# Kernel optimization log

Measured on AMD Instinct MI355X. Metric: run time of the kernel, lower is better.

Reference implementation:

```python
import jax, jax.numpy as jnp
import numpy as np
from jax import lax

PI = float(np.pi)
K_TOP = 128
N_BINS = 64

def _normalize(x, axis, eps=1e-12):
    n = jnp.sqrt(jnp.sum(x * x, axis=axis, keepdims=True))
    return x / jnp.maximum(n, eps)

def _conv(x, w, b):
    y = lax.conv_general_dilated(x, w, (1, 1), 'SAME',
                                 dimension_numbers=('NCHW', 'OIHW', 'NCHW'))
    return y + b[None, :, None, None]

def _maxpool2(x):
    return lax.reduce_window(x, -jnp.inf, lax.max, (1, 1, 2, 2), (1, 1, 2, 2), 'VALID')

def setup_inputs() -> dict:
    key = jax.random.key(0)
    ks = jax.random.split(key, 12)
    B, C, H, W = 16, 1, 512, 512
    PD, NPT = 128, 64
    fc_in = NPT + 64 * 4 * 4 + 3  # 1091
    def lin_init(k, fan_in, shape):
        bound = 1.0 / np.sqrt(fan_in)
        return jax.random.uniform(k, shape, jnp.float32, -bound, bound)
    return {
        'image': jax.random.normal(ks[0], (B, C, H, W), jnp.float32),
        'pattern_receptors': jax.random.normal(ks[1], (NPT, PD), jnp.float32) * 0.1,
        'conv1_w': lin_init(ks[2], 2 * 9, (32, 2, 3, 3)),
        'conv1_b': lin_init(ks[3], 2 * 9, (32,)),
        'conv2_w': lin_init(ks[4], 32 * 9, (64, 32, 3, 3)),
        'conv2_b': lin_init(ks[5], 32 * 9, (64,)),
        'fc1_w': lin_init(ks[6], fc_in, (512, fc_in)),
        'fc1_b': lin_init(ks[7], fc_in, (512,)),
        'fc2_w': lin_init(ks[8], 512, (PD, 512)),
        'fc2_b': lin_init(ks[9], 512, (PD,)),
        'ln_g': jnp.ones((PD,), jnp.float32),
        'ln_b': jnp.zeros((PD,), jnp.float32),
    }

def reference(image, pattern_receptors, conv1_w, conv1_b, conv2_w, conv2_b,
              fc1_w, fc1_b, fc2_w, fc2_b, ln_g, ln_b):
    B, C, H, W = image.shape
    # ---- frequency domain ----
    freq = jnp.fft.fft2(image, axes=(2, 3))
    magnitude = jnp.abs(freq)
    phase = jnp.angle(freq)
    # ---- pattern matching (topk of FFT magnitude vs receptor library) ----
    flat_mag = magnitude.reshape(B, C, -1)
    dom, _ = lax.top_k(flat_mag, K_TOP)          # [B, C, 128]
    dom = dom.reshape(B, -1)                     # [B, C*128]
    sims = jnp.matmul(_normalize(dom, 1), _normalize(pattern_receptors, 1).T)  # [B, 64]
    # ---- spatial path (original detaches via numpy roundtrip) ----
    img = lax.stop_gradient(image)
    gy = jnp.gradient(img, axis=2)
    gx = jnp.gradient(img, axis=3)
    gmag = jnp.sqrt(gx * gx + gy * gy)
    gori = jnp.arctan2(gy, gx)
    spat_in = jnp.stack([gmag, gori], axis=2).reshape(B, 2 * C, H, W)
    h = jax.nn.relu(_conv(spat_in, conv1_w, conv1_b))
    h = _maxpool2(h)                             # [B,32,H/2,W/2]
    h = jax.nn.relu(_conv(h, conv2_w, conv2_b))  # [B,64,H/2,W/2]
    Hp, Wp = h.shape[2], h.shape[3]
    h = h.reshape(B, 64, 4, Hp // 4, 4, Wp // 4).mean(axis=(3, 5))  # adaptive avg 4x4
    spatial = h.reshape(B, -1)                   # [B, 1024]
    # ---- phase statistics ----
    pf = phase.reshape(B, -1)
    p_mean = jnp.mean(pf, axis=1)
    p_std = jnp.std(pf, axis=1, ddof=1)
    bins = jnp.clip(jnp.floor((pf + PI) / (2 * PI) * N_BINS), 0, N_BINS - 1).astype(jnp.int32)
    hist = jnp.zeros((B, N_BINS), jnp.float32).at[jnp.arange(B)[:, None], bins].add(1.0)
    hist = hist / jnp.sum(hist, axis=1, keepdims=True)
    p_ent = -jnp.sum(hist * jnp.log(hist + 1e-10), axis=1)
    phase_feats = jnp.stack([p_mean, p_std, p_ent], axis=1)  # [B, 3]
    # ---- fuse: MLP + LayerNorm ----
    combined = jnp.concatenate([sims, spatial, phase_feats], axis=1)  # [B, 1091]
    z = jax.nn.relu(combined @ fc1_w.T + fc1_b)
    z = z @ fc2_w.T + fc2_b
    mu = jnp.mean(z, axis=-1, keepdims=True)
    var = jnp.var(z, axis=-1, keepdims=True)
    holo = (z - mu) / jnp.sqrt(var + 1e-5) * ln_g + ln_b
    return sims, spatial, phase_feats, holo
```

## Files before the change

kernel.cpp:

```cpp
#include <hip/hip_runtime.h>
#include <hip/hip_fp16.h>
#include <math.h>


#define PI_F 3.14159274f
#define TWO_PI_F 6.28318548f

typedef _Float16 half8 __attribute__((ext_vector_type(8)));
typedef float floatx4 __attribute__((ext_vector_type(4)));

#define OFF_BIG   8388608
#define OFF_SMALL 25165824
#define NBIN 2048

__global__ void __launch_bounds__(256) init_kernel(float* __restrict__ zp,
                                                   float2* __restrict__ tw,
                                                   const float* __restrict__ w2,
                                                   const float* __restrict__ w1,
                                                   _Float16* __restrict__ wrep,
                                                   _Float16* __restrict__ w1r) {
    int idx = blockIdx.x * 256 + threadIdx.x;
    if (idx < 82992) zp[idx] = 0.0f;
    if (idx < 512) {
        if (idx == 0) tw[0] = make_float2(1.f, 0.f);
        else {
            int h = 31 - __clz(idx);
            int H = 1 << h;
            float sn, cs;
            sincosf(-PI_F * (float)(idx - H) / (float)H, &sn, &cs);
            tw[idx] = make_float2(cs, sn);
        }
    }
    if (idx < 18432) {
        int j = idx & 7;
        int lane = (idx >> 3) & 63;
        int nt = (idx >> 9) & 3;
        int tap = idx >> 11;
        int oc = nt * 16 + (lane & 15);
        int ic = (lane >> 4) * 8 + j;
        wrep[idx] = (_Float16)w2[(oc * 32 + ic) * 9 + tap];
    }
    if (idx < 1024) {
        int j = idx & 7;
        int lane = (idx >> 3) & 63;
        int nt = idx >> 9;
        int oc = nt * 16 + (lane & 15);
        int k = (lane >> 4) * 8 + j;
        _Float16 v = (_Float16)0.f;
        if (k < 18) {
            int tap = k >> 1, ch = k & 1;
            v = (_Float16)w1[oc * 18 + ch * 9 + tap];
        }
        w1r[idx] = v;
    }
}

__global__ void __launch_bounds__(256) fft_rows(const float* __restrict__ img,
                                                const float2* __restrict__ twg,
                                                float2* __restrict__ rowfft) {
    __shared__ float2 s[512];
    __shared__ float2 tw[512];
    const int t = threadIdx.x;
    const int row = blockIdx.x;
    const float* x = img + (long long)row * 512;

    for (int i = t; i < 512; i += 256) tw[i] = twg[i];
    for (int i = t; i < 512; i += 256) s[i] = make_float2(x[i], 0.f);
    __syncthreads();
#pragma unroll
    for (int st = 9; st >= 1; --st) {
        const int half = 1 << (st - 1);
        const int pos = t & (half - 1);
        const int grp = t >> (st - 1);
        const int i1 = (grp << st) + pos;
        const int i2 = i1 + half;
        float2 w = tw[half + pos];
        float2 a = s[i1], b = s[i2];
        float dx = a.x - b.x, dy = a.y - b.y;
        s[i1] = make_float2(a.x + b.x, a.y + b.y);
        s[i2] = make_float2(dx * w.x - dy * w.y, dx * w.y + dy * w.x);
        __syncthreads();
    }
    for (int i = t; i < 512; i += 256) rowfft[(long long)row * 512 + i] = s[i];
}

__global__ void __launch_bounds__(256) fft_cols(const float2* __restrict__ rowfft,
                                                const float2* __restrict__ twg,
                                                float* __restrict__ magT,
                                                float* __restrict__ psum,
                                                float* __restrict__ psumsq,
                                                unsigned* __restrict__ phist,
                                                unsigned* __restrict__ mhist) {
    __shared__ float2 s[8 * 512];
    __shared__ float2 tw[512];
    __shared__ unsigned ph[64];
    __shared__ unsigned mh[NBIN];
    __shared__ float red[8];
    const int t = threadIdx.x;
    const int b = blockIdx.x >> 6;
    const int x0 = (blockIdx.x & 63) * 8;

    for (int i = t; i < 512; i += 256) tw[i] = twg[i];
    if (t < 64) ph[t] = 0u;
    for (int i = t; i < NBIN; i += 256) mh[i] = 0u;
    for (int idx = t; idx < 8 * 512; idx += 256) {
        int y = idx >> 3;
        int c = idx & 7;
        s[c * 512 + y] = rowfft[((long long)(b * 512 + y)) * 512 + x0 + c];
    }
    __syncthreads();

    const int c = t >> 5;
    const int j0 = t & 31;
    float2* sc = s + c * 512;
#pragma unroll
    for (int st = 9; st >= 1; --st) {
        const int half = 1 << (st - 1);
#pragma unroll
        for (int k = 0; k < 8; ++k) {
            int j = j0 + (k << 5);
            int pos = j & (half - 1);
            int grp = j >> (st - 1);
            int i1 = (grp << st) + pos;
            int i2 = i1 + half;
            float2 w = tw[half + pos];
            float2 a = sc[i1], bb = sc[i2];
            float dx = a.x - bb.x, dy = a.y - bb.y;
            sc[i1] = make_float2(a.x + bb.x, a.y + bb.y);
            sc[i2] = make_float2(dx * w.x - dy * w.y, dx * w.y + dy * w.x);
        }
        __syncthreads();
    }

    float lsum = 0.f, lsq = 0.f;
    for (int idx = t; idx < 8 * 512; idx += 256) {
        int cc = idx >> 9;
        int y = idx & 511;
        float2 v = s[cc * 512 + y];
        float mag = sqrtf(v.x * v.x + v.y * v.y);
        magT[((long long)(b * 512 + x0 + cc)) * 512 + y] = mag;
        unsigned mb = min(__float_as_uint(mag) >> 20, (unsigned)(NBIN - 1));
        atomicAdd(&mh[mb], 1u);
        float phv = atan2f(v.y, v.x);
        lsum += phv;
        lsq += phv * phv;
        int bin = (int)floorf((phv + PI_F) / TWO_PI_F * 64.0f);
        bin = min(max(bin, 0), 63);
        atomicAdd(&ph[bin], 1u);
    }
    for (int off = 32; off > 0; off >>= 1) {
        lsum += __shfl_down(lsum, off);
        lsq  += __shfl_down(lsq, off);
    }
    if ((t & 63) == 0) { red[t >> 6] = lsum; red[4 + (t >> 6)] = lsq; }
    __syncthreads();
    if (t == 0) {
        atomicAdd(psum + b,   red[0] + red[1] + red[2] + red[3]);
        atomicAdd(psumsq + b, red[4] + red[5] + red[6] + red[7]);
    }
    if (t < 64 && ph[t]) atomicAdd(&phist[b * 64 + t], ph[t]);
    for (int i = t; i < NBIN; i += 256)
        if (mh[i]) atomicAdd(&mhist[b * NBIN + i], mh[i]);
}

__global__ void __launch_bounds__(256) thresh_kernel(const unsigned* __restrict__ mhist,
                                                     int* __restrict__ selbin) {
    __shared__ unsigned csum[256];
    const int b = blockIdx.x, t = threadIdx.x;
    unsigned s = 0;
    for (int i = 0; i < NBIN / 256; ++i) s += mhist[b * NBIN + t * (NBIN / 256) + i];
    csum[t] = s;
    __syncthreads();
    if (t == 0) {
        unsigned acc = 0; int chunk = 0;
        for (int i = 255; i >= 0; --i) {
            acc += csum[i];
            if (acc >= 128u) { chunk = i; break; }
        }
        unsigned acc2 = acc - csum[chunk];
        int tb = chunk * (NBIN / 256);
        for (int i = chunk * (NBIN / 256) + (NBIN / 256) - 1; i >= chunk * (NBIN / 256); --i) {
            acc2 += mhist[b * NBIN + i];
            if (acc2 >= 128u) { tb = i; break; }
        }
        selbin[b] = tb;
    }
}

#define TK_CAP 4096
__global__ void __launch_bounds__(256) collect_kernel(const float* __restrict__ magT,
                                                      const int* __restrict__ selbin,
                                                      float* __restrict__ cand,
                                                      unsigned* __restrict__ ccnt) {
    const int blk = blockIdx.x;
    const int b = blk >> 4, chunk = blk & 15;
    const unsigned tb = (unsigned)selbin[b];
    const floatx4* m = (const floatx4*)(magT + (long long)b * 262144 + chunk * 16384);
    float* cb = cand + b * TK_CAP;
    for (int i = threadIdx.x; i < 4096; i += 256) {
        floatx4 v = m[i];
#pragma unroll
        for (int k = 0; k < 4; ++k) {
            float x = v[k];
            unsigned bin = min(__float_as_uint(x) >> 20, (unsigned)(NBIN - 1));
            if (bin >= tb) {
                unsigned p = atomicAdd(&ccnt[b], 1u);
                if (p < TK_CAP) cb[p] = x;
            }
        }
    }
}

__global__ void __launch_bounds__(1024) sort_kernel(const float* __restrict__ cand,
                                                    const unsigned* __restrict__ ccnt,
                                                    float* __restrict__ dom) {
    __shared__ float c[TK_CAP];
    const int b = blockIdx.x, t = threadIdx.x;
    const unsigned n = min(ccnt[b], (unsigned)TK_CAP);
    int P = 256;
    while (P < (int)n) P <<= 1;
    for (int i = t; i < P; i += 1024) c[i] = (i < (int)n) ? cand[b * TK_CAP + i] : -1.0f;
    __syncthreads();
    for (int k = 2; k <= P; k <<= 1) {
        for (int j = k >> 1; j > 0; j >>= 1) {
            for (int i = t; i < P; i += 1024) {
                int ixj = i ^ j;
                if (ixj > i) {
                    float a = c[i], d = c[ixj];
                    bool up = ((i & k) == 0);
                    if (up ? (a < d) : (a > d)) { c[i] = d; c[ixj] = a; }
                }
            }
            __syncthreads();
        }
    }
    if (t < 128) dom[b * 128 + t] = c[t];
}

__global__ void __launch_bounds__(256) sims_kernel(const float* __restrict__ dom,
                                                   const float* __restrict__ rec,
                                                   float* __restrict__ comb,
                                                   float* __restrict__ dout) {
    __shared__ float sd[16 * 128];
    __shared__ float sr[64 * 128];
    __shared__ float scale[80];
    const int t = threadIdx.x;
    for (int i = t; i < 2048; i += 256) sd[i] = dom[i];
    for (int i = t; i < 8192; i += 256) sr[i] = rec[i];
    __syncthreads();
    if (t < 80) {
        const float* base = (t < 16) ? (sd + t * 128) : (sr + (t - 16) * 128);
        float s = 0.f;
        for (int k = 0; k < 128; ++k) s += base[k] * base[k];
        scale[t] = 1.0f / fmaxf(sqrtf(s), 1e-12f);
    }
    __syncthreads();
    for (int o = t; o < 1024; o += 256) {
        int b = o >> 6, p = o & 63;
        const float* dv = sd + b * 128;
        const float* rv = sr + p * 128;
        float s = 0.f;
        for (int k = 0; k < 128; ++k) s += dv[k] * rv[k];
        float val = s * scale[b] * scale[16 + p];
        dout[b * 64 + p] = val;
        comb[b * 1091 + p] = val;
    }
}

__global__ void __launch_bounds__(256) grad_conv1_mfma(const float* __restrict__ img,
                                                       const half8* __restrict__ w1r,
                                                       const float* __restrict__ c1b,
                                                       _Float16* __restrict__ h1) {
    __shared__ float simg[36 * 37];
    __shared__ _Float16 sgrad[(34 * 36 + 1) * 2];
    const int blk = blockIdx.x;
    const int b = blk >> 8;
    const int tr = blk & 255;
    const int TY = (tr >> 4) * 32, TX = (tr & 15) * 32;
    const int t = threadIdx.x;
    const float* im = img + (long long)b * 262144;

    for (int idx = t; idx < 1296; idx += 256) {
        int iy = idx / 36, ix = idx - iy * 36;
        int gy = min(max(TY - 2 + iy, 0), 511);
        int gx = min(max(TX - 2 + ix, 0), 511);
        simg[iy * 37 + ix] = im[gy * 512 + gx];
    }
    if (t == 0) { sgrad[2448] = (_Float16)0.f; sgrad[2449] = (_Float16)0.f; }
    __syncthreads();

    for (int idx = t; idx < 1156; idx += 256) {
        int ly = idx / 34, lx = idx - ly * 34;
        int gy = TY - 1 + ly, gx = TX - 1 + lx;
        float up = simg[ly * 37 + lx + 1];
        float dn = simg[(ly + 2) * 37 + lx + 1];
        float lf = simg[(ly + 1) * 37 + lx];
        float rt = simg[(ly + 1) * 37 + lx + 2];
        float fy = (gy <= 0 || gy >= 511) ? 1.f : 0.5f;
        float fx = (gx <= 0 || gx >= 511) ? 1.f : 0.5f;
        float gyv = (dn - up) * fy, gxv = (rt - lf) * fx;
        bool inside = ((unsigned)gy < 512u) && ((unsigned)gx < 512u);
        float mag = inside ? sqrtf(gxv * gxv + gyv * gyv) : 0.f;
        float ori = inside ? atan2f(gyv, gxv) : 0.f;
        int p = (ly * 36 + lx) * 2;
        sgrad[p] = (_Float16)mag;
        sgrad[p + 1] = (_Float16)ori;
    }
    __syncthreads();

    const int w = t >> 6, lane = t & 63;
    const int q = lane >> 4, m = lane & 15;
    const int oc0 = m, oc1 = 16 + m;
    const float bias0 = c1b[oc0], bias1 = c1b[oc1];
    half8 Bf0 = w1r[lane], Bf1 = w1r[64 + lane];
    const unsigned* gp = (const unsigned*)sgrad;
    const int ZP = 1224;

    const int sy = (m >> 1) & 1, sx = m & 1, dqx = m >> 2;

#pragma unroll 4
    for (int i = 0; i < 16; ++i) {
        const int mt = w * 16 + i;
        const int qy = mt >> 2, qxg = mt & 3;
        const int py = 2 * qy + sy;
        const int px = 2 * (qxg * 4 + dqx) + sx;
        const int base = py * 36 + px;

        int o0 = (q == 0) ? base      : (q == 1) ? base + 37 : (q == 2) ? base + 74 : ZP;
        int o1 = (q == 0) ? base + 1  : (q == 1) ? base + 38 : ZP;
        int o2 = (q == 0) ? base + 2  : (q == 1) ? base + 72 : ZP;
        int o3 = (q == 0) ? base + 36 : (q == 1) ? base + 73 : ZP;

        union { unsigned u[4]; half8 h; } Af;
        Af.u[0] = gp[o0]; Af.u[1] = gp[o1]; Af.u[2] = gp[o2]; Af.u[3] = gp[o3];

        floatx4 acc0 = {bias0, bias0, bias0, bias0};
        floatx4 acc1 = {bias1, bias1, bias1, bias1};
        acc0 = __builtin_amdgcn_mfma_f32_16x16x32_f16(Af.h, Bf0, acc0, 0, 0, 0);
        acc1 = __builtin_amdgcn_mfma_f32_16x16x32_f16(Af.h, Bf1, acc1, 0, 0, 0);

        float v0 = fmaxf(fmaxf(acc0[0], acc0[1]), fmaxf(acc0[2], acc0[3]));
        float v1 = fmaxf(fmaxf(acc1[0], acc1[1]), fmaxf(acc1[2], acc1[3]));
        v0 = fmaxf(v0, 0.f);
        v1 = fmaxf(v1, 0.f);

        const int PY = (TY >> 1) + qy;
        const int PX = (TX >> 1) + qxg * 4 + q;
        _Float16* dst = h1 + (((size_t)(b * 256 + PY)) * 256 + PX) * 32;
        dst[oc0] = (_Float16)v0;
        dst[oc1] = (_Float16)v1;
    }
}

__global__ void __launch_bounds__(256) conv2_mfma(const _Float16* __restrict__ h1,
                                                  const _Float16* __restrict__ wrep,
                                                  const float* __restrict__ c2b,
                                                  float* __restrict__ sacc) {
    __shared__ _Float16 tile[18 * 34 * 32];
    __shared__ float lsum[64];
    const int blk = blockIdx.x;
    const int b  = blk >> 7;
    const int yt = (blk >> 3) & 15;
    const int xt = blk & 7;
    const int y0 = yt * 16, x0 = xt * 32;
    const int t = threadIdx.x;
    if (t < 64) lsum[t] = 0.f;

    for (int c = t; c < 18 * 136; c += 256) {
        int row = c / 136;
        int chunk = c - row * 136;
        int gy = y0 - 1 + row;
        int px = chunk >> 2;
        int gx = x0 - 1 + px;
        floatx4 v = {0.f, 0.f, 0.f, 0.f};
        if ((unsigned)gy < 256u && (unsigned)gx < 256u)
            v = *(const floatx4*)(h1 + (((size_t)(b * 256 + gy)) * 256 + gx) * 32 + (chunk & 3) * 8);
        *(floatx4*)(tile + (row * 34 + px) * 32 + (chunk & 3) * 8) = v;
    }
    __syncthreads();

    const int w = t >> 6, lane = t & 63;
    const int q = lane >> 4, ln15 = lane & 15;
    float bias[4];
#pragma unroll
    for (int nt = 0; nt < 4; ++nt) bias[nt] = c2b[nt * 16 + ln15];
    float partial[4] = {0.f, 0.f, 0.f, 0.f};

#pragma unroll 1
    for (int gr = 0; gr < 2; ++gr) {
        floatx4 acc[4][4];
#pragma unroll
        for (int mt = 0; mt < 4; ++mt)
#pragma unroll
            for (int nt = 0; nt < 4; ++nt)
                acc[mt][nt] = floatx4{bias[nt], bias[nt], bias[nt], bias[nt]};

        const _Float16* ab = tile + (((w * 4 + gr * 2) * 34) + ln15) * 32 + q * 8;
        const _Float16* wk = wrep + lane * 8;

#pragma unroll 1
        for (int ky = 0; ky < 3; ++ky) {
#pragma unroll
            for (int kx = 0; kx < 3; ++kx) {
                half8 Bf[4];
#pragma unroll
                for (int nt = 0; nt < 4; ++nt)
                    Bf[nt] = *(const half8*)(wk + (kx * 4 + nt) * 512);
#pragma unroll
                for (int mt = 0; mt < 4; ++mt) {
                    half8 Af = *(const half8*)(ab + (mt >> 1) * 1088 + (mt & 1) * 512 + kx * 32);
#pragma unroll
                    for (int nt = 0; nt < 4; ++nt)
                        acc[mt][nt] = __builtin_amdgcn_mfma_f32_16x16x32_f16(Af, Bf[nt], acc[mt][nt], 0, 0, 0);
                }
            }
            ab += 34 * 32;
            wk += 3 * 2048;
        }

#pragma unroll
        for (int mt = 0; mt < 4; ++mt)
#pragma unroll
            for (int nt = 0; nt < 4; ++nt)
#pragma unroll
                for (int rg = 0; rg < 4; ++rg)
                    partial[nt] += fmaxf(acc[mt][nt][rg], 0.f);
    }

#pragma unroll
    for (int nt = 0; nt < 4; ++nt) {
        float v = partial[nt];
        v += __shfl_xor(v, 16);
        v += __shfl_xor(v, 32);
        if (lane < 16) atomicAdd(&lsum[nt * 16 + ln15], v);
    }
    __syncthreads();
    const int cell = (yt >> 2) * 4 + (xt >> 1);
    if (t < 64) atomicAdd(&sacc[(((b << 6) + t) << 4) + cell], lsum[t]);
}

__global__ void __launch_bounds__(256) finalize_kernel(const float* __restrict__ sacc,
                                                       const float* __restrict__ psum,
                                                       const float* __restrict__ psumsq,
                                                       const unsigned* __restrict__ phist,
                                                       float* __restrict__ comb,
                                                       float* __restrict__ dout) {
    if (blockIdx.x < 64) {
        int idx = blockIdx.x * 256 + threadIdx.x;
        int b = idx >> 10, j = idx & 1023;
        float v = sacc[idx] * (1.0f / 4096.0f);
        dout[1024 + idx] = v;
        comb[b * 1091 + 64 + j] = v;
    } else {
        int t = threadIdx.x;
        if (t < 16) {
            const float N = 262144.f;
            float s = psum[t];
            float mean = s / N;
            float var = (psumsq[t] - s * s / N) / (N - 1.f);
            float sd = sqrtf(fmaxf(var, 0.f));
            float ent = 0.f;
            for (int i = 0; i < 64; ++i) {
                float p = (float)phist[t * 64 + i] / N;
                ent -= p * logf(p + 1e-10f);
            }
            dout[17408 + t * 3 + 0] = mean;
            dout[17408 + t * 3 + 1] = sd;
            dout[17408 + t * 3 + 2] = ent;
            float* cb = comb + t * 1091 + 1088;
            cb[0] = mean; cb[1] = sd; cb[2] = ent;
        }
    }
}

__global__ void __launch_bounds__(256) fc1_kernel(const float* __restrict__ comb,
                                                  const float* __restrict__ W1,
                                                  const float* __restrict__ B1,
                                                  float* __restrict__ out1) {
    const int wid = blockIdx.x * 4 + (threadIdx.x >> 6);
    const int lane = threadIdx.x & 63;
    const int b = wid >> 9, o = wid & 511;
    const float* w = W1 + (size_t)o * 1091;
    const float* c = comb + b * 1091;
    float acc = 0.f;
#pragma unroll 4
    for (int i = 0; i < 17; ++i) {
        int k = i * 64 + lane;
        acc += w[k] * c[k];
    }
    if (lane < 3) acc += w[1088 + lane] * c[1088 + lane];
#pragma unroll
    for (int off = 32; off > 0; off >>= 1) acc += __shfl_down(acc, off);
    if (lane == 0) out1[b * 512 + o] = fmaxf(acc + B1[o], 0.f);
}

__global__ void __launch_bounds__(256) fc2_kernel(const float* __restrict__ out1,
                                                  const float* __restrict__ W2,
                                                  const float* __restrict__ B2,
                                                  float* __restrict__ z) {
    const int wid = blockIdx.x * 4 + (threadIdx.x >> 6);
    const int lane = threadIdx.x & 63;
    const int b = wid >> 7, o = wid & 127;
    const float* w = W2 + (size_t)o * 512;
    const float* c = out1 + b * 512;
    float acc = 0.f;
#pragma unroll
    for (int i = 0; i < 8; ++i) {
        int k = i * 64 + lane;
        acc += w[k] * c[k];
    }
#pragma unroll
    for (int off = 32; off > 0; off >>= 1) acc += __shfl_down(acc, off);
    if (lane == 0) z[b * 128 + o] = acc + B2[o];
}

__global__ void __launch_bounds__(128) ln_kernel(const float* __restrict__ z,
                                                 const float* __restrict__ g,
                                                 const float* __restrict__ beta,
                                                 float* __restrict__ dout) {
    __shared__ float red[4];
    const int b = blockIdx.x, t = threadIdx.x;
    float acc = z[b * 128 + t];
    float s = acc;
    for (int off = 32; off > 0; off >>= 1) s += __shfl_down(s, off);
    if ((t & 63) == 0) red[t >> 6] = s;
    __syncthreads();
    float mu = (red[0] + red[1]) * (1.0f / 128.0f);
    float d = acc - mu;
    float q = d * d;
    for (int off = 32; off > 0; off >>= 1) q += __shfl_down(q, off);
    if ((t & 63) == 0) red[2 + (t >> 6)] = q;
    __syncthreads();
    float var = (red[2] + red[3]) * (1.0f / 128.0f);
    dout[17456 + b * 128 + t] = d / sqrtf(var + 1e-5f) * g[t] + beta[t];
}

extern "C" void kernel_launch(void* const* d_in, const int* in_sizes, int n_in,
                              void* d_out, int out_size, void* d_ws, size_t ws_size,
                              hipStream_t stream) {
    const float* img = (const float*)d_in[0];
    const float* rec = (const float*)d_in[1];
    const float* w1  = (const float*)d_in[2];
    const float* c1b = (const float*)d_in[3];
    const float* w2  = (const float*)d_in[4];
    const float* c2b = (const float*)d_in[5];
    const float* fw1 = (const float*)d_in[6];
    const float* fb1 = (const float*)d_in[7];
    const float* fw2 = (const float*)d_in[8];
    const float* fb2 = (const float*)d_in[9];
    const float* lng = (const float*)d_in[10];
    const float* lnb = (const float*)d_in[11];
    float* out = (float*)d_out;

    float* ws = (float*)d_ws;
    float2* rowfft = (float2*)ws;
    float* magT    = ws + OFF_BIG;
    _Float16* h1   = (_Float16*)(ws + OFF_BIG);
    float* small_  = ws + OFF_SMALL;
    float* sacc    = small_;
    float* psum    = small_ + 16384;
    float* psumsq  = small_ + 16400;
    unsigned* phist = (unsigned*)(small_ + 16416);
    unsigned* mhist = (unsigned*)(small_ + 17440);
    unsigned* ccnt  = (unsigned*)(small_ + 82976);
    int* selbin    = (int*)(small_ + 82992);
    float* dom     = small_ + 83008;
    float* comb    = small_ + 85056;
    float* out1    = small_ + 102512;
    _Float16* wrep = (_Float16*)(small_ + 110704);
    float2* twg    = (float2*)(small_ + 119920);
    float* cand    = small_ + 120944;
    float* zbuf    = cand;
    _Float16* w1r  = (_Float16*)(small_ + 186480);

    init_kernel<<<325, 256, 0, stream>>>(sacc, twg, w2, w1, wrep, w1r);
    fft_rows<<<8192, 256, 0, stream>>>(img, twg, rowfft);
    fft_cols<<<1024, 256, 0, stream>>>(rowfft, twg, magT, psum, psumsq, phist, mhist);
    thresh_kernel<<<16, 256, 0, stream>>>(mhist, selbin);
    collect_kernel<<<256, 256, 0, stream>>>(magT, selbin, cand, ccnt);
    sort_kernel<<<16, 1024, 0, stream>>>(cand, ccnt, dom);
    sims_kernel<<<1, 256, 0, stream>>>(dom, rec, comb, out);
    grad_conv1_mfma<<<4096, 256, 0, stream>>>(img, (const half8*)w1r, c1b, h1);
    conv2_mfma<<<2048, 256, 0, stream>>>(h1, wrep, c2b, sacc);
    finalize_kernel<<<65, 256, 0, stream>>>(sacc, psum, psumsq, phist, comb, out);
    fc1_kernel<<<2048, 256, 0, stream>>>(comb, fw1, fb1, out1);
    fc2_kernel<<<512, 256, 0, stream>>>(out1, fw2, fb2, zbuf);
    ln_kernel<<<16, 128, 0, stream>>>(zbuf, lng, lnb, out);
}
```

Baseline: 333.4 us.

## Pack two real rows per complex FFT and store intermediates in fp16

```diff
diff --git a/kernel.cpp b/kernel.cpp
--- a/kernel.cpp
+++ b/kernel.cpp
@@ -7,6 +7,7 @@
 #define TWO_PI_F 6.28318548f
 
 typedef _Float16 half8 __attribute__((ext_vector_type(8)));
+typedef _Float16 h2 __attribute__((ext_vector_type(2)));
 typedef float floatx4 __attribute__((ext_vector_type(4)));
 
 #define OFF_BIG   8388608
@@ -55,17 +56,18 @@
     }
 }
 
-__global__ void __launch_bounds__(256) fft_rows(const float* __restrict__ img,
-                                                const float2* __restrict__ twg,
-                                                float2* __restrict__ rowfft) {
+__global__ void __launch_bounds__(256) fft_rows2(const float* __restrict__ img,
+                                                 const float2* __restrict__ twg,
+                                                 h2* __restrict__ rowhf) {
     __shared__ float2 s[512];
     __shared__ float2 tw[512];
     const int t = threadIdx.x;
-    const int row = blockIdx.x;
-    const float* x = img + (long long)row * 512;
+    const long long rbase = (long long)blockIdx.x * 1024;
+    const float* x0 = img + rbase;
+    const float* x1 = x0 + 512;
 
     for (int i = t; i < 512; i += 256) tw[i] = twg[i];
-    for (int i = t; i < 512; i += 256) s[i] = make_float2(x[i], 0.f);
+    for (int i = t; i < 512; i += 256) s[i] = make_float2(x0[i], x1[i]);
     __syncthreads();
 #pragma unroll
     for (int st = 9; st >= 1; --st) {
@@ -81,12 +83,21 @@
         s[i2] = make_float2(dx * w.x - dy * w.y, dx * w.y + dy * w.x);
         __syncthreads();
     }
-    for (int i = t; i < 512; i += 256) rowfft[(long long)row * 512 + i] = s[i];
-}
-
-__global__ void __launch_bounds__(256) fft_cols(const float2* __restrict__ rowfft,
+    for (int i = t; i < 512; i += 256) {
+        int k = __brev((unsigned)i) >> 23;
+        int kp = (512 - k) & 511;
+        int jp = __brev((unsigned)kp) >> 23;
+        float2 Z = s[i], Zp = s[jp];
+        rowhf[rbase + i]       = h2{(_Float16)(0.5f * (Z.x + Zp.x)),
+                                    (_Float16)(0.5f * (Z.y - Zp.y))};
+        rowhf[rbase + 512 + i] = h2{(_Float16)(0.5f * (Z.y + Zp.y)),
+                                    (_Float16)(-0.5f * (Z.x - Zp.x))};
+    }
+}
+
+__global__ void __launch_bounds__(256) fft_cols(const h2* __restrict__ rowhf,
                                                 const float2* __restrict__ twg,
-                                                float* __restrict__ magT,
+                                                _Float16* __restrict__ magT,
                                                 float* __restrict__ psum,
                                                 float* __restrict__ psumsq,
                                                 unsigned* __restrict__ phist,
@@ -106,7 +117,8 @@
     for (int idx = t; idx < 8 * 512; idx += 256) {
         int y = idx >> 3;
         int c = idx & 7;
-        s[c * 512 + y] = rowfft[((long long)(b * 512 + y)) * 512 + x0 + c];
+        h2 v = rowhf[((long long)(b * 512 + y)) * 512 + x0 + c];
+        s[c * 512 + y] = make_float2((float)v[0], (float)v[1]);
     }
     __syncthreads();
 
@@ -138,8 +150,10 @@
         int y = idx & 511;
         float2 v = s[cc * 512 + y];
         float mag = sqrtf(v.x * v.x + v.y * v.y);
-        magT[((long long)(b * 512 + x0 + cc)) * 512 + y] = mag;
-        unsigned mb = min(__float_as_uint(mag) >> 20, (unsigned)(NBIN - 1));
+        union { _Float16 h; unsigned short u; } cvt;
+        cvt.h = (_Float16)mag;
+        magT[((long long)(b * 512 + x0 + cc)) * 512 + y] = cvt.h;
+        unsigned mb = min((unsigned)(cvt.u >> 4), (unsigned)(NBIN - 1));
         atomicAdd(&mh[mb], 1u);
         float phv = atan2f(v.y, v.x);
         lsum += phv;
@@ -188,24 +202,32 @@
 }
 
 #define TK_CAP 4096
-__global__ void __launch_bounds__(256) collect_kernel(const float* __restrict__ magT,
+__global__ void __launch_bounds__(256) collect_kernel(const _Float16* __restrict__ magT,
                                                       const int* __restrict__ selbin,
                                                       float* __restrict__ cand,
                                                       unsigned* __restrict__ ccnt) {
     const int blk = blockIdx.x;
     const int b = blk >> 4, chunk = blk & 15;
     const unsigned tb = (unsigned)selbin[b];
-    const floatx4* m = (const floatx4*)(magT + (long long)b * 262144 + chunk * 16384);
+    const uint4* m = (const uint4*)(magT + (size_t)b * 262144 + chunk * 16384);
     float* cb = cand + b * TK_CAP;
-    for (int i = threadIdx.x; i < 4096; i += 256) {
-        floatx4 v = m[i];
-#pragma unroll
-        for (int k = 0; k < 4; ++k) {
-            float x = v[k];
-            unsigned bin = min(__float_as_uint(x) >> 20, (unsigned)(NBIN - 1));
-            if (bin >= tb) {
-                unsigned p = atomicAdd(&ccnt[b], 1u);
-                if (p < TK_CAP) cb[p] = x;
+    for (int i = threadIdx.x; i < 2048; i += 256) {
+        uint4 v4 = m[i];
+        unsigned vv[4] = {v4.x, v4.y, v4.z, v4.w};
+#pragma unroll
+        for (int j = 0; j < 4; ++j) {
+#pragma unroll
+            for (int k = 0; k < 2; ++k) {
+                unsigned short ub = (k == 0) ? (unsigned short)(vv[j] & 0xFFFFu)
+                                             : (unsigned short)(vv[j] >> 16);
+                if ((unsigned)(ub >> 4) >= tb) {
+                    unsigned p = atomicAdd(&ccnt[b], 1u);
+                    if (p < TK_CAP) {
+                        union { unsigned short u; _Float16 h; } c2;
+                        c2.u = ub;
+                        cb[p] = (float)c2.h;
+                    }
+                }
             }
         }
     }
@@ -553,9 +575,9 @@
     float* out = (float*)d_out;
 
     float* ws = (float*)d_ws;
-    float2* rowfft = (float2*)ws;
-    float* magT    = ws + OFF_BIG;
-    _Float16* h1   = (_Float16*)(ws + OFF_BIG);
+    h2* rowhf       = (h2*)ws;
+    _Float16* magT  = (_Float16*)(ws + OFF_BIG);
+    _Float16* h1    = (_Float16*)(ws + OFF_BIG);
     float* small_  = ws + OFF_SMALL;
     float* sacc    = small_;
     float* psum    = small_ + 16384;
@@ -574,8 +596,8 @@
     _Float16* w1r  = (_Float16*)(small_ + 186480);
 
     init_kernel<<<325, 256, 0, stream>>>(sacc, twg, w2, w1, wrep, w1r);
-    fft_rows<<<8192, 256, 0, stream>>>(img, twg, rowfft);
-    fft_cols<<<1024, 256, 0, stream>>>(rowfft, twg, magT, psum, psumsq, phist, mhist);
+    fft_rows2<<<4096, 256, 0, stream>>>(img, twg, rowhf);
+    fft_cols<<<1024, 256, 0, stream>>>(rowhf, twg, magT, psum, psumsq, phist, mhist);
     thresh_kernel<<<16, 256, 0, stream>>>(mhist, selbin);
     collect_kernel<<<256, 256, 0, stream>>>(magT, selbin, cand, ccnt);
     sort_kernel<<<16, 1024, 0, stream>>>(cand, ccnt, dom);
```

Measured after the change: 297.7 us. 1.12x faster.
